# Optimization experiments

Hardware: AMD Instinct MI355X
Metric: run time of the kernel (lower is better)

## Reference

```python
import jax, jax.numpy as jnp
import numpy as np

IN_DIM = 1024
OUT_DIM = 1024
NHEAD = 16
K = 9  # template(1032) - dim(1024) + 1


def _slinear(vec, template, conv_w, conv_b, lin_b):
    # Conv2d over template produces the [out_dim, in_dim] weight matrix.
    w = jax.lax.conv_general_dilated(
        template, conv_w, window_strides=(1, 1), padding='VALID',
        dimension_numbers=('NCHW', 'OIHW', 'NCHW'))  # [1,1,out_dim,in_dim]
    w = w[0, 0] + conv_b  # broadcast conv bias (scalar per out-channel)
    return vec @ w.T + lin_b  # F.linear(vec, w) + bias


def setup_inputs() -> dict:
    key = jax.random.key(0)
    ks = jax.random.split(key, 13)
    S, B = 2048, 2
    d = {
        'query': jax.random.normal(ks[0], (S, B, IN_DIM), jnp.float32),
        'key': jax.random.normal(ks[1], (S, B, IN_DIM), jnp.float32),
        'value': jax.random.normal(ks[2], (S, B, IN_DIM), jnp.float32),
        'template': jax.random.normal(ks[3], (1, 1, 1032, 1032), jnp.float32),
    }
    for i, name in enumerate(['wq', 'wk', 'wv']):
        d[name + '_cw'] = jax.random.normal(ks[4 + 3 * i], (1, 1, K, K), jnp.float32) * 0.05
        d[name + '_cb'] = jax.random.normal(ks[5 + 3 * i], (1,), jnp.float32) * 0.05
        d[name + '_b'] = jax.random.normal(ks[6 + 3 * i], (OUT_DIM,), jnp.float32) * 0.05
    return d


def reference(query, key, value, template,
              wq_cw, wq_cb, wq_b, wk_cw, wk_cb, wk_b, wv_cw, wv_cb, wv_b):
    q = _slinear(query, template, wq_cw, wq_cb, wq_b)
    k = _slinear(key, template, wk_cw, wk_cb, wk_b)
    v = _slinear(value, template, wv_cw, wv_cb, wv_b)
    S, B = q.shape[0], q.shape[1]
    h_dim = OUT_DIM // NHEAD
    scale = h_dim ** 0.5
    qh = q.reshape(S, B, NHEAD, h_dim)
    kh = k.reshape(S, B, NHEAD, h_dim)
    vh = v.reshape(S, B, NHEAD, h_dim)
    # batch_first=False path: scores then softmax over last dim
    scores = jnp.einsum('ibhd,jbhd->bhij', qh, kh) / scale  # [B,H,S,S]
    attn = jax.nn.softmax(scores, axis=-1)
    out = jnp.einsum('bhij,jbhd->ibhd', attn, vh).reshape(S, B, OUT_DIM)
    return out
```

## Files before the change

kernel.cpp:

```cpp
#include <hip/hip_runtime.h>
#include <math.h>

#define TDIM   1032
#define DIM    1024
#define SLEN   2048
#define BATCH  2
#define NROWS  (SLEN*BATCH)
#define NHEAD  16
#define HD     64

typedef unsigned short u16;
typedef short short8 __attribute__((ext_vector_type(8)));
typedef short bf16x4 __attribute__((ext_vector_type(4)));
typedef float f32x4  __attribute__((ext_vector_type(4)));

#define CSCALE 0.18033688011112042f

__device__ inline unsigned fbits(float x) {
    union { float f; unsigned u; } v; v.f = x; return v.u;
}
__device__ inline float asfloat(unsigned u) {
    union { unsigned u; float f; } v; v.u = u; return v.f;
}
__device__ inline u16 f2bf_rne(float x) {
    unsigned u = fbits(x);
    unsigned r = u + 0x7fffu + ((u >> 16) & 1u);
    return (u16)(r >> 16);
}
__device__ inline float bf2f(u16 b) { return asfloat(((unsigned)b) << 16); }
__device__ inline void dma16(const u16* g, u16* l) {
    __builtin_amdgcn_global_load_lds(
        (const __attribute__((address_space(1))) void*)g,
        (__attribute__((address_space(3))) void*)l, 16, 0, 0);
}

__global__ __launch_bounds__(256) void conv_weight_kernel(
    const float* __restrict__ tmpl,
    const float* __restrict__ cw0, const float* __restrict__ cb0,
    const float* __restrict__ cw1, const float* __restrict__ cb1,
    const float* __restrict__ cw2, const float* __restrict__ cb2,
    u16* __restrict__ Wh, u16* __restrict__ Wl)
{
    int t = blockIdx.z;
    const float* cw = (t == 0) ? cw0 : ((t == 1) ? cw1 : cw2);
    const float* cb = (t == 0) ? cb0 : ((t == 1) ? cb1 : cb2);
    __shared__ float scw[81];
    if (threadIdx.x < 81) scw[threadIdx.x] = cw[threadIdx.x];
    __syncthreads();
    int i = blockIdx.x * 256 + threadIdx.x;
    int o4 = blockIdx.y * 4;
    float cbv = cb[0];
    float acc[4] = {cbv, cbv, cbv, cbv};
    #pragma unroll
    for (int ry = 0; ry < 12; ++ry) {
        const float* trow = tmpl + (size_t)(o4 + ry) * TDIM + i;
        float tv[9];
        #pragma unroll
        for (int dx = 0; dx < 9; ++dx) tv[dx] = trow[dx];
        #pragma unroll
        for (int oo = 0; oo < 4; ++oo) {
            int dy = ry - oo;
            if (dy >= 0 && dy <= 8) {
                #pragma unroll
                for (int dx = 0; dx < 9; ++dx)
                    acc[oo] = fmaf(scw[dy * 9 + dx], tv[dx], acc[oo]);
            }
        }
    }
    #pragma unroll
    for (int oo = 0; oo < 4; ++oo) {
        size_t idx = (size_t)t * DIM * DIM + (size_t)(o4 + oo) * DIM + i;
        u16 h = f2bf_rne(acc[oo]);
        Wh[idx] = h;
        Wl[idx] = f2bf_rne(acc[oo] - bf2f(h));
    }
}

__global__ __launch_bounds__(256, 3) void qkv_mfma_gemm(
    const float* __restrict__ x0, const float* __restrict__ x1,
    const float* __restrict__ x2,
    const u16* __restrict__ Whg, const u16* __restrict__ Wlg,
    const float* __restrict__ b0, const float* __restrict__ b1,
    const float* __restrict__ b2,
    u16* __restrict__ Qh, u16* __restrict__ Ql,
    u16* __restrict__ Kh, u16* __restrict__ Kl,
    u16* __restrict__ Vb)
{
    unsigned flat = blockIdx.x + 8u * blockIdx.y + 256u * blockIdx.z;
    unsigned swz = (flat & 7u) * 96u + (flat >> 3);
    int t = swz >> 8;
    int n0 = (swz & 7u) * 128;
    int m0 = ((swz >> 3) & 31u) * 128;

    const float* X    = (t == 0) ? x0 : ((t == 1) ? x1 : x2);
    const u16* Bh_g   = Whg + (size_t)t * DIM * DIM;
    const u16* Bl_g   = Wlg + (size_t)t * DIM * DIM;
    const float* bias = (t == 0) ? b0 : ((t == 1) ? b1 : b2);

    __shared__ __align__(16) u16 lds[16384];
    u16* sAh = lds;
    u16* sAl = lds + 4096;
    u16* sBh = lds + 8192;
    u16* sBl = lds + 12288;

    int tid = threadIdx.x;
    int w = tid >> 6, lane = tid & 63;
    int c = lane & 15, quad = lane >> 4;
    int mh = (w >> 1) * 64, nh = (w & 1) * 64;

    int arow = w * 32 + (lane & 31);
    int acol = (lane >> 5) * 16;
    const float* aptr = X + (size_t)(m0 + arow) * DIM + acol;

    int srow = lane >> 2, sgr = lane & 3;

    f32x4 acc[4][4];
    #pragma unroll
    for (int i = 0; i < 4; ++i)
        #pragma unroll
        for (int j = 0; j < 4; ++j)
            #pragma unroll
            for (int r = 0; r < 4; ++r) acc[i][j][r] = 0.0f;

    float bias_v[4];
    #pragma unroll
    for (int tn = 0; tn < 4; ++tn) bias_v[tn] = bias[n0 + nh + tn * 16 + c];

    float4 xa[4];
    #pragma unroll
    for (int i = 0; i < 2; ++i) {
        int rb = w * 32 + i * 16;
        const u16* gh = Bh_g + (size_t)(n0 + rb + srow) * DIM + sgr * 8;
        const u16* gl = Bl_g + (size_t)(n0 + rb + srow) * DIM + sgr * 8;
        dma16(gh, sBh + rb * 32);
        dma16(gl, sBl + rb * 32);
    }
    #pragma unroll
    for (int j = 0; j < 4; ++j) xa[j] = *(const float4*)(aptr + j * 4);

    for (int it = 0; it < 32; ++it) {
        #pragma unroll
        for (int g = 0; g < 2; ++g) {
            float v[8] = { xa[2*g].x, xa[2*g].y, xa[2*g].z, xa[2*g].w,
                           xa[2*g+1].x, xa[2*g+1].y, xa[2*g+1].z, xa[2*g+1].w };
            short8 hv, lv;
            #pragma unroll
            for (int e = 0; e < 8; ++e) {
                unsigned u = fbits(v[e]);
                hv[e] = (short)(u >> 16);
                float l = v[e] - asfloat(u & 0xffff0000u);
                lv[e] = (short)(fbits(l) >> 16);
            }
            *(short8*)(sAh + arow * 32 + acol + g * 8) = hv;
            *(short8*)(sAl + arow * 32 + acol + g * 8) = lv;
        }
        __syncthreads();

        short8 ah[4], al[4], bh[4], bl[4];
        #pragma unroll
        for (int tt = 0; tt < 4; ++tt) {
            int mi = (mh + tt * 16 + c) * 32 + quad * 8;
            ah[tt] = *(short8*)(sAh + mi);
            al[tt] = *(short8*)(sAl + mi);
            int ni = (nh + tt * 16 + c) * 32 + quad * 8;
            bh[tt] = *(short8*)(sBh + ni);
            bl[tt] = *(short8*)(sBl + ni);
        }
        __syncthreads();

        if (it < 31) {
            int kg = (it + 1) * 4;
            #pragma unroll
            for (int i = 0; i < 2; ++i) {
                int rb = w * 32 + i * 16;
                const u16* gh = Bh_g + (size_t)(n0 + rb + srow) * DIM + (kg + sgr) * 8;
                const u16* gl = Bl_g + (size_t)(n0 + rb + srow) * DIM + (kg + sgr) * 8;
                dma16(gh, sBh + rb * 32);
                dma16(gl, sBl + rb * 32);
            }
            #pragma unroll
            for (int j = 0; j < 4; ++j)
                xa[j] = *(const float4*)(aptr + (it + 1) * 32 + j * 4);
        }

        #pragma unroll
        for (int tm = 0; tm < 4; ++tm)
            #pragma unroll
            for (int tn = 0; tn < 4; ++tn) {
                acc[tm][tn] = __builtin_amdgcn_mfma_f32_16x16x32_bf16(
                    ah[tm], bh[tn], acc[tm][tn], 0, 0, 0);
                acc[tm][tn] = __builtin_amdgcn_mfma_f32_16x16x32_bf16(
                    ah[tm], bl[tn], acc[tm][tn], 0, 0, 0);
                acc[tm][tn] = __builtin_amdgcn_mfma_f32_16x16x32_bf16(
                    al[tm], bh[tn], acc[tm][tn], 0, 0, 0);
            }
    }

    if (t < 2) {
        u16* Yh = (t == 0) ? Qh : Kh;
        u16* Yl = (t == 0) ? Ql : Kl;
        float qs = (t == 0) ? CSCALE : 1.0f;
        #pragma unroll
        for (int tm = 0; tm < 4; ++tm)
            #pragma unroll
            for (int r = 0; r < 4; ++r) {
                int m = m0 + mh + tm * 16 + quad * 4 + r;
                #pragma unroll
                for (int tn = 0; tn < 4; ++tn) {
                    int n = n0 + nh + tn * 16 + c;
                    float o = (acc[tm][tn][r] + bias_v[tn]) * qs;
                    unsigned bo = fbits(o);
                    Yh[(size_t)m * DIM + n] = (u16)(bo >> 16);
                    float l = o - asfloat(bo & 0xffff0000u);
                    Yl[(size_t)m * DIM + n] = (u16)(fbits(l) >> 16);
                }
            }
    } else {
        #pragma unroll
        for (int tm = 0; tm < 4; ++tm)
            #pragma unroll
            for (int r = 0; r < 4; ++r) {
                int m = m0 + mh + tm * 16 + quad * 4 + r;
                #pragma unroll
                for (int tn = 0; tn < 4; ++tn) {
                    int n = n0 + nh + tn * 16 + c;
                    Vb[(size_t)m * DIM + n] =
                        (u16)(fbits(acc[tm][tn][r] + bias_v[tn]) >> 16);
                }
            }
    }
}

__global__ __launch_bounds__(256) void vt_kernel(
    const u16* __restrict__ Vb, u16* __restrict__ Vt)
{
    int b = blockIdx.z, h = blockIdx.y, s0 = blockIdx.x * 64;
    __shared__ __align__(16) u16 tile[64][80];
    int tid = threadIdx.x;
    int sl = tid >> 2, d0 = (tid & 3) * 16;
    const u16* src = Vb + (size_t)((s0 + sl) * BATCH + b) * DIM + h * HD + d0;
    short8 v0 = *(const short8*)src;
    short8 v1 = *(const short8*)(src + 8);
    #pragma unroll
    for (int j = 0; j < 8; ++j) {
        tile[d0 + j][sl] = (u16)v0[j];
        tile[d0 + 8 + j][sl] = (u16)v1[j];
    }
    __syncthreads();
    int d = tid >> 2, sc0 = (tid & 3) * 16;
    u16* dst = Vt + (size_t)((b * NHEAD + h) * HD + d) * SLEN + s0 + sc0;
    *(short8*)dst = *(const short8*)&tile[d][sc0];
    *(short8*)(dst + 8) = *(const short8*)&tile[d][sc0 + 8];
}

__global__ __launch_bounds__(256, 3) void attn_mfma_kernel(
    const u16* __restrict__ Qh, const u16* __restrict__ Ql,
    const u16* __restrict__ Kh, const u16* __restrict__ Kl,
    const u16* __restrict__ Vt, float* __restrict__ out)
{
    unsigned flat = blockIdx.x + 16u * blockIdx.y + 256u * blockIdx.z;
    unsigned swz = (flat & 7u) * 64u + (flat >> 3);
    int q0 = (swz & 15u) * 128;
    int h = (swz >> 4) & 15u;
    int b = swz >> 8;

    int tid = threadIdx.x;
    int w = tid >> 6, lane = tid & 63;
    int c = lane & 15, quad = lane >> 4;

    __shared__ __align__(16) u16 sbuf[2][3][4096];

    short8 qhf[2][2], qlf[2][2];
    #pragma unroll
    for (int u = 0; u < 2; ++u) {
        int s = q0 + w * 32 + u * 16 + c;
        size_t base = (size_t)(s * BATCH + b) * DIM + h * HD + quad * 8;
        qhf[u][0] = *(const short8*)(Qh + base);
        qhf[u][1] = *(const short8*)(Qh + base + 32);
        qlf[u][0] = *(const short8*)(Ql + base);
        qlf[u][1] = *(const short8*)(Ql + base + 32);
    }

    f32x4 acc[2][4];
    #pragma unroll
    for (int u = 0; u < 2; ++u)
        #pragma unroll
        for (int i = 0; i < 4; ++i)
            #pragma unroll
            for (int r = 0; r < 4; ++r) acc[u][i][r] = 0.0f;
    float m_run[2] = {-1e38f, -1e38f}, l_run[2] = {0.0f, 0.0f};

    int r3 = lane >> 3, c3 = lane & 7;
    int sw = c3 ^ r3;
    const size_t bhofs = (size_t)(b * NHEAD + h) * HD;

    #define ISSUE_DMA(n0v, bufv) do {                                          \
        _Pragma("unroll")                                                      \
        for (int j = 0; j < 2; ++j) {                                          \
            int i_ = 2 * w + j;                                                \
            int row_ = i_ * 8 + r3;                                            \
            size_t gk = (size_t)(((n0v) + row_) * BATCH + b) * DIM + h * HD + sw * 8; \
            dma16(Kh + gk, &sbuf[bufv][0][i_ * 512]);                          \
            dma16(Kl + gk, &sbuf[bufv][1][i_ * 512]);                          \
            size_t gv = (bhofs + row_) * SLEN + (n0v) + sw * 8;                \
            dma16(Vt + gv, &sbuf[bufv][2][i_ * 512]);                          \
        }                                                                      \
    } while (0)

    ISSUE_DMA(0, 0);

    for (int it = 0; it < 32; ++it) {
        int cur = it & 1;
        __syncthreads();
        if (it < 31) ISSUE_DMA((it + 1) * 64, cur ^ 1);

        const u16* bKh = sbuf[cur][0];
        const u16* bKl = sbuf[cur][1];
        const u16* bVt = sbuf[cur][2];

        f32x4 sc[2][4];
        #pragma unroll
        for (int ct = 0; ct < 4; ++ct) {
            int row = ct * 16 + c, rw = row & 7;
            int kb = row * 64;
            short8 kh0 = *(const short8*)(bKh + kb + ((quad ^ rw) * 8));
            short8 kh1 = *(const short8*)(bKh + kb + (((4 + quad) ^ rw) * 8));
            short8 kl0 = *(const short8*)(bKl + kb + ((quad ^ rw) * 8));
            short8 kl1 = *(const short8*)(bKl + kb + (((4 + quad) ^ rw) * 8));
            __builtin_amdgcn_s_setprio(1);
            #pragma unroll
            for (int u = 0; u < 2; ++u) {
                f32x4 s = {0.0f, 0.0f, 0.0f, 0.0f};
                s = __builtin_amdgcn_mfma_f32_16x16x32_bf16(kh0, qhf[u][0], s, 0, 0, 0);
                s = __builtin_amdgcn_mfma_f32_16x16x32_bf16(kh1, qhf[u][1], s, 0, 0, 0);
                s = __builtin_amdgcn_mfma_f32_16x16x32_bf16(kh0, qlf[u][0], s, 0, 0, 0);
                s = __builtin_amdgcn_mfma_f32_16x16x32_bf16(kh1, qlf[u][1], s, 0, 0, 0);
                s = __builtin_amdgcn_mfma_f32_16x16x32_bf16(kl0, qhf[u][0], s, 0, 0, 0);
                s = __builtin_amdgcn_mfma_f32_16x16x32_bf16(kl1, qhf[u][1], s, 0, 0, 0);
                sc[u][ct] = s;
            }
            __builtin_amdgcn_s_setprio(0);
        }

        short8 pf[2][2];
        #pragma unroll
        for (int u = 0; u < 2; ++u) {
            float pm = sc[u][0][0];
            #pragma unroll
            for (int ct = 0; ct < 4; ++ct)
                #pragma unroll
                for (int r = 0; r < 4; ++r)
                    pm = fmaxf(pm, sc[u][ct][r]);
            pm = fmaxf(pm, __shfl_xor(pm, 16));
            pm = fmaxf(pm, __shfl_xor(pm, 32));
            float mnew = fmaxf(m_run[u], pm);
            bool noresc = __all(pm <= m_run[u]);
            if (!noresc) {
                float al = exp2f(m_run[u] - mnew);
                float alr[4];
                #pragma unroll
                for (int r = 0; r < 4; ++r)
                    alr[r] = __shfl(al, (lane & 48) | (quad * 4 + r));
                #pragma unroll
                for (int ctd = 0; ctd < 4; ++ctd)
                    #pragma unroll
                    for (int r = 0; r < 4; ++r) acc[u][ctd][r] *= alr[r];
                l_run[u] *= al;
            }
            m_run[u] = mnew;

            float ps = 0.0f;
            unsigned pw[8];
            #pragma unroll
            for (int ct = 0; ct < 4; ++ct) {
                float p0 = exp2f(sc[u][ct][0] - mnew);
                float p1 = exp2f(sc[u][ct][1] - mnew);
                float p2 = exp2f(sc[u][ct][2] - mnew);
                float p3 = exp2f(sc[u][ct][3] - mnew);
                ps += (p0 + p1) + (p2 + p3);
                pw[2*ct]   = (fbits(p0) >> 16) | (fbits(p1) & 0xffff0000u);
                pw[2*ct+1] = (fbits(p2) >> 16) | (fbits(p3) & 0xffff0000u);
            }
            ps += __shfl_xor(ps, 16);
            ps += __shfl_xor(ps, 32);
            l_run[u] += ps;

            int sl0 = c + ((quad & 1) << 5);
            int sl1 = sl0 + 16;
            int sel = quad >> 1;
            union W8 { unsigned wv[4]; short8 s8; } f0, f1;
            {
                unsigned a0 = __shfl(pw[0], sl0), a1 = __shfl(pw[2], sl0);
                f0.wv[0] = sel ? a1 : a0;
                unsigned b0 = __shfl(pw[1], sl0), b1 = __shfl(pw[3], sl0);
                f0.wv[1] = sel ? b1 : b0;
                unsigned c0 = __shfl(pw[0], sl1), c1 = __shfl(pw[2], sl1);
                f0.wv[2] = sel ? c1 : c0;
                unsigned d0 = __shfl(pw[1], sl1), d1 = __shfl(pw[3], sl1);
                f0.wv[3] = sel ? d1 : d0;
                unsigned e0 = __shfl(pw[4], sl0), e1 = __shfl(pw[6], sl0);
                f1.wv[0] = sel ? e1 : e0;
                unsigned g0 = __shfl(pw[5], sl0), g1 = __shfl(pw[7], sl0);
                f1.wv[1] = sel ? g1 : g0;
                unsigned h0 = __shfl(pw[4], sl1), h1 = __shfl(pw[6], sl1);
                f1.wv[2] = sel ? h1 : h0;
                unsigned i0 = __shfl(pw[5], sl1), i1 = __shfl(pw[7], sl1);
                f1.wv[3] = sel ? i1 : i0;
            }
            pf[u][0] = f0.s8;
            pf[u][1] = f1.s8;
        }

        #pragma unroll
        for (int ctd = 0; ctd < 4; ++ctd) {
            int vrow = ctd * 16 + c, vrw = vrow & 7;
            int vb = vrow * 64;
            short8 v0 = *(const short8*)(bVt + vb + ((quad ^ vrw) * 8));
            short8 v1 = *(const short8*)(bVt + vb + (((4 + quad) ^ vrw) * 8));
            __builtin_amdgcn_s_setprio(1);
            #pragma unroll
            for (int u = 0; u < 2; ++u) {
                acc[u][ctd] = __builtin_amdgcn_mfma_f32_16x16x32_bf16(
                    pf[u][0], v0, acc[u][ctd], 0, 0, 0);
                acc[u][ctd] = __builtin_amdgcn_mfma_f32_16x16x32_bf16(
                    pf[u][1], v1, acc[u][ctd], 0, 0, 0);
            }
            __builtin_amdgcn_s_setprio(0);
        }
    }
    #undef ISSUE_DMA

    #pragma unroll
    for (int u = 0; u < 2; ++u) {
        float rl[4];
        #pragma unroll
        for (int r = 0; r < 4; ++r)
            rl[r] = 1.0f / __shfl(l_run[u], (lane & 48) | (quad * 4 + r));
        #pragma unroll
        for (int ctd = 0; ctd < 4; ++ctd)
            #pragma unroll
            for (int r = 0; r < 4; ++r) {
                int s = q0 + w * 32 + u * 16 + quad * 4 + r;
                out[(size_t)(s * BATCH + b) * DIM + h * HD + ctd * 16 + c] =
                    acc[u][ctd][r] * rl[r];
            }
    }
}

extern "C" void kernel_launch(void* const* d_in, const int* in_sizes, int n_in,
                              void* d_out, int out_size, void* d_ws, size_t ws_size,
                              hipStream_t stream)
{
    const float* query = (const float*)d_in[0];
    const float* key_  = (const float*)d_in[1];
    const float* value = (const float*)d_in[2];
    const float* tmpl  = (const float*)d_in[3];
    const float* wq_cw = (const float*)d_in[4];
    const float* wq_cb = (const float*)d_in[5];
    const float* wq_b  = (const float*)d_in[6];
    const float* wk_cw = (const float*)d_in[7];
    const float* wk_cb = (const float*)d_in[8];
    const float* wk_b  = (const float*)d_in[9];
    const float* wv_cw = (const float*)d_in[10];
    const float* wv_cb = (const float*)d_in[11];
    const float* wv_b  = (const float*)d_in[12];

    char* ws = (char*)d_ws;
    u16* Wh = (u16*)(ws);
    u16* Wl = (u16*)(ws + 6291456);
    u16* Qh = (u16*)(ws + 12582912);
    u16* Ql = (u16*)(ws + 20971520);
    u16* Kh = (u16*)(ws + 29360128);
    u16* Kl = (u16*)(ws + 37748736);
    u16* Vb = (u16*)(ws + 46137344);
    u16* Vt = (u16*)(ws + 54525952);
    float* out = (float*)d_out;

    conv_weight_kernel<<<dim3(DIM / 256, DIM / 4, 3), 256, 0, stream>>>(
        tmpl, wq_cw, wq_cb, wk_cw, wk_cb, wv_cw, wv_cb, Wh, Wl);

    qkv_mfma_gemm<<<dim3(DIM / 128, NROWS / 128, 3), 256, 0, stream>>>(
        query, key_, value, Wh, Wl, wq_b, wk_b, wv_b, Qh, Ql, Kh, Kl, Vb);

    vt_kernel<<<dim3(SLEN / 64, NHEAD, BATCH), 256, 0, stream>>>(Vb, Vt);

    attn_mfma_kernel<<<dim3(SLEN / 128, NHEAD, BATCH), 256, 0, stream>>>(
        Qh, Ql, Kh, Kl, Vt, out);
}
```

Baseline: 321.7 us.

## Use 8 waves per attention block with 16 query rows each

The attention kernel now launches 512 threads per block, so each of 8 waves handles a single 16-row query tile instead of two. Each wave issues one K/V DMA chunk instead of two, and all V fragments are loaded from LDS before the softmax so the PV MFMAs run back to back under raised priority. This lowers per-thread register use to allow more waves per CU and better latency hiding. In exchange, each K/V fragment read from LDS now feeds fewer MFMAs, and the barrier spans more waves.

```diff
diff --git a/kernel.cpp b/kernel.cpp
--- a/kernel.cpp
+++ b/kernel.cpp
@@ -253,7 +253,7 @@
     *(short8*)(dst + 8) = *(const short8*)&tile[d][sc0 + 8];
 }
 
-__global__ __launch_bounds__(256, 3) void attn_mfma_kernel(
+__global__ __launch_bounds__(512, 4) void attn_mfma_kernel(
     const u16* __restrict__ Qh, const u16* __restrict__ Ql,
     const u16* __restrict__ Kh, const u16* __restrict__ Kl,
     const u16* __restrict__ Vt, float* __restrict__ out)
@@ -270,41 +270,34 @@
 
     __shared__ __align__(16) u16 sbuf[2][3][4096];
 
-    short8 qhf[2][2], qlf[2][2];
-    #pragma unroll
-    for (int u = 0; u < 2; ++u) {
-        int s = q0 + w * 32 + u * 16 + c;
+    short8 qhf[2], qlf[2];
+    {
+        int s = q0 + w * 16 + c;
         size_t base = (size_t)(s * BATCH + b) * DIM + h * HD + quad * 8;
-        qhf[u][0] = *(const short8*)(Qh + base);
-        qhf[u][1] = *(const short8*)(Qh + base + 32);
-        qlf[u][0] = *(const short8*)(Ql + base);
-        qlf[u][1] = *(const short8*)(Ql + base + 32);
-    }
-
-    f32x4 acc[2][4];
-    #pragma unroll
-    for (int u = 0; u < 2; ++u)
-        #pragma unroll
-        for (int i = 0; i < 4; ++i)
-            #pragma unroll
-            for (int r = 0; r < 4; ++r) acc[u][i][r] = 0.0f;
-    float m_run[2] = {-1e38f, -1e38f}, l_run[2] = {0.0f, 0.0f};
+        qhf[0] = *(const short8*)(Qh + base);
+        qhf[1] = *(const short8*)(Qh + base + 32);
+        qlf[0] = *(const short8*)(Ql + base);
+        qlf[1] = *(const short8*)(Ql + base + 32);
+    }
+
+    f32x4 acc[4];
+    #pragma unroll
+    for (int i = 0; i < 4; ++i)
+        #pragma unroll
+        for (int r = 0; r < 4; ++r) acc[i][r] = 0.0f;
+    float m_run = -1e38f, l_run = 0.0f;
 
     int r3 = lane >> 3, c3 = lane & 7;
     int sw = c3 ^ r3;
     const size_t bhofs = (size_t)(b * NHEAD + h) * HD;
 
     #define ISSUE_DMA(n0v, bufv) do {                                          \
-        _Pragma("unroll")                                                      \
-        for (int j = 0; j < 2; ++j) {                                          \
-            int i_ = 2 * w + j;                                                \
-            int row_ = i_ * 8 + r3;                                            \
-            size_t gk = (size_t)(((n0v) + row_) * BATCH + b) * DIM + h * HD + sw * 8; \
-            dma16(Kh + gk, &sbuf[bufv][0][i_ * 512]);                          \
-            dma16(Kl + gk, &sbuf[bufv][1][i_ * 512]);                          \
-            size_t gv = (bhofs + row_) * SLEN + (n0v) + sw * 8;                \
-            dma16(Vt + gv, &sbuf[bufv][2][i_ * 512]);                          \
-        }                                                                      \
+        int row_ = w * 8 + r3;                                                 \
+        size_t gk = (size_t)(((n0v) + row_) * BATCH + b) * DIM + h * HD + sw * 8; \
+        dma16(Kh + gk, &sbuf[bufv][0][w * 512]);                               \
+        dma16(Kl + gk, &sbuf[bufv][1][w * 512]);                               \
+        size_t gv = (bhofs + row_) * SLEN + (n0v) + sw * 8;                    \
+        dma16(Vt + gv, &sbuf[bufv][2][w * 512]);                               \
     } while (0)
 
     ISSUE_DMA(0, 0);
@@ -318,7 +311,7 @@
         const u16* bKl = sbuf[cur][1];
         const u16* bVt = sbuf[cur][2];
 
-        f32x4 sc[2][4];
+        f32x4 sc[4];
         #pragma unroll
         for (int ct = 0; ct < 4; ++ct) {
             int row = ct * 16 + c, rw = row & 7;
@@ -328,35 +321,40 @@
             short8 kl0 = *(const short8*)(bKl + kb + ((quad ^ rw) * 8));
             short8 kl1 = *(const short8*)(bKl + kb + (((4 + quad) ^ rw) * 8));
             __builtin_amdgcn_s_setprio(1);
-            #pragma unroll
-            for (int u = 0; u < 2; ++u) {
-                f32x4 s = {0.0f, 0.0f, 0.0f, 0.0f};
-                s = __builtin_amdgcn_mfma_f32_16x16x32_bf16(kh0, qhf[u][0], s, 0, 0, 0);
-                s = __builtin_amdgcn_mfma_f32_16x16x32_bf16(kh1, qhf[u][1], s, 0, 0, 0);
-                s = __builtin_amdgcn_mfma_f32_16x16x32_bf16(kh0, qlf[u][0], s, 0, 0, 0);
-                s = __builtin_amdgcn_mfma_f32_16x16x32_bf16(kh1, qlf[u][1], s, 0, 0, 0);
-                s = __builtin_amdgcn_mfma_f32_16x16x32_bf16(kl0, qhf[u][0], s, 0, 0, 0);
-                s = __builtin_amdgcn_mfma_f32_16x16x32_bf16(kl1, qhf[u][1], s, 0, 0, 0);
-                sc[u][ct] = s;
-            }
+            f32x4 s = {0.0f, 0.0f, 0.0f, 0.0f};
+            s = __builtin_amdgcn_mfma_f32_16x16x32_bf16(kh0, qhf[0], s, 0, 0, 0);
+            s = __builtin_amdgcn_mfma_f32_16x16x32_bf16(kh1, qhf[1], s, 0, 0, 0);
+            s = __builtin_amdgcn_mfma_f32_16x16x32_bf16(kh0, qlf[0], s, 0, 0, 0);
+            s = __builtin_amdgcn_mfma_f32_16x16x32_bf16(kh1, qlf[1], s, 0, 0, 0);
+            s = __builtin_amdgcn_mfma_f32_16x16x32_bf16(kl0, qhf[0], s, 0, 0, 0);
+            s = __builtin_amdgcn_mfma_f32_16x16x32_bf16(kl1, qhf[1], s, 0, 0, 0);
             __builtin_amdgcn_s_setprio(0);
-        }
-
-        short8 pf[2][2];
-        #pragma unroll
-        for (int u = 0; u < 2; ++u) {
-            float pm = sc[u][0][0];
+            sc[ct] = s;
+        }
+
+        short8 vv[4][2];
+        #pragma unroll
+        for (int ctd = 0; ctd < 4; ++ctd) {
+            int vrow = ctd * 16 + c, vrw = vrow & 7;
+            int vb = vrow * 64;
+            vv[ctd][0] = *(const short8*)(bVt + vb + ((quad ^ vrw) * 8));
+            vv[ctd][1] = *(const short8*)(bVt + vb + (((4 + quad) ^ vrw) * 8));
+        }
+
+        short8 pf0, pf1;
+        {
+            float pm = sc[0][0];
             #pragma unroll
             for (int ct = 0; ct < 4; ++ct)
                 #pragma unroll
                 for (int r = 0; r < 4; ++r)
-                    pm = fmaxf(pm, sc[u][ct][r]);
+                    pm = fmaxf(pm, sc[ct][r]);
             pm = fmaxf(pm, __shfl_xor(pm, 16));
             pm = fmaxf(pm, __shfl_xor(pm, 32));
-            float mnew = fmaxf(m_run[u], pm);
-            bool noresc = __all(pm <= m_run[u]);
+            float mnew = fmaxf(m_run, pm);
+            bool noresc = __all(pm <= m_run);
             if (!noresc) {
-                float al = exp2f(m_run[u] - mnew);
+                float al = exp2f(m_run - mnew);
                 float alr[4];
                 #pragma unroll
                 for (int r = 0; r < 4; ++r)
@@ -364,26 +362,26 @@
                 #pragma unroll
                 for (int ctd = 0; ctd < 4; ++ctd)
                     #pragma unroll
-                    for (int r = 0; r < 4; ++r) acc[u][ctd][r] *= alr[r];
-                l_run[u] *= al;
-            }
-            m_run[u] = mnew;
+                    for (int r = 0; r < 4; ++r) acc[ctd][r] *= alr[r];
+                l_run *= al;
+            }
+            m_run = mnew;
 
             float ps = 0.0f;
             unsigned pw[8];
             #pragma unroll
             for (int ct = 0; ct < 4; ++ct) {
-                float p0 = exp2f(sc[u][ct][0] - mnew);
-                float p1 = exp2f(sc[u][ct][1] - mnew);
-                float p2 = exp2f(sc[u][ct][2] - mnew);
-                float p3 = exp2f(sc[u][ct][3] - mnew);
+                float p0 = exp2f(sc[ct][0] - mnew);
+                float p1 = exp2f(sc[ct][1] - mnew);
+                float p2 = exp2f(sc[ct][2] - mnew);
+                float p3 = exp2f(sc[ct][3] - mnew);
                 ps += (p0 + p1) + (p2 + p3);
                 pw[2*ct]   = (fbits(p0) >> 16) | (fbits(p1) & 0xffff0000u);
                 pw[2*ct+1] = (fbits(p2) >> 16) | (fbits(p3) & 0xffff0000u);
             }
             ps += __shfl_xor(ps, 16);
             ps += __shfl_xor(ps, 32);
-            l_run[u] += ps;
+            l_run += ps;
 
             int sl0 = c + ((quad & 1) << 5);
             int sl1 = sl0 + 16;
@@ -407,42 +405,34 @@
                 unsigned i0 = __shfl(pw[5], sl1), i1 = __shfl(pw[7], sl1);
                 f1.wv[3] = sel ? i1 : i0;
             }
-            pf[u][0] = f0.s8;
-            pf[u][1] = f1.s8;
-        }
-
+            pf0 = f0.s8;
+            pf1 = f1.s8;
+        }
+
+        __builtin_amdgcn_s_setprio(1);
         #pragma unroll
         for (int ctd = 0; ctd < 4; ++ctd) {
-            int vrow = ctd * 16 + c, vrw = vrow & 7;
-            int vb = vrow * 64;
-            short8 v0 = *(const short8*)(bVt + vb + ((quad ^ vrw) * 8));
-            short8 v1 = *(const short8*)(bVt + vb + (((4 + quad) ^ vrw) * 8));
-            __builtin_amdgcn_s_setprio(1);
-            #pragma unroll
-            for (int u = 0; u < 2; ++u) {
-                acc[u][ctd] = __builtin_amdgcn_mfma_f32_16x16x32_bf16(
-                    pf[u][0], v0, acc[u][ctd], 0, 0, 0);
-                acc[u][ctd] = __builtin_amdgcn_mfma_f32_16x16x32_bf16(
-                    pf[u][1], v1, acc[u][ctd], 0, 0, 0);
-            }
-            __builtin_amdgcn_s_setprio(0);
-        }
+            acc[ctd] = __builtin_amdgcn_mfma_f32_16x16x32_bf16(
+                pf0, vv[ctd][0], acc[ctd], 0, 0, 0);
+            acc[ctd] = __builtin_amdgcn_mfma_f32_16x16x32_bf16(
+                pf1, vv[ctd][1], acc[ctd], 0, 0, 0);
+        }
+        __builtin_amdgcn_s_setprio(0);
     }
     #undef ISSUE_DMA
 
-    #pragma unroll
-    for (int u = 0; u < 2; ++u) {
+    {
         float rl[4];
         #pragma unroll
         for (int r = 0; r < 4; ++r)
-            rl[r] = 1.0f / __shfl(l_run[u], (lane & 48) | (quad * 4 + r));
+            rl[r] = 1.0f / __shfl(l_run, (lane & 48) | (quad * 4 + r));
         #pragma unroll
         for (int ctd = 0; ctd < 4; ++ctd)
             #pragma unroll
             for (int r = 0; r < 4; ++r) {
-                int s = q0 + w * 32 + u * 16 + quad * 4 + r;
+                int s = q0 + w * 16 + quad * 4 + r;
                 out[(size_t)(s * BATCH + b) * DIM + h * HD + ctd * 16 + c] =
-                    acc[u][ctd][r] * rl[r];
+                    acc[ctd][r] * rl[r];
             }
     }
 }
@@ -484,6 +474,6 @@
 
     vt_kernel<<<dim3(SLEN / 64, NHEAD, BATCH), 256, 0, stream>>>(Vb, Vt);
 
-    attn_mfma_kernel<<<dim3(SLEN / 128, NHEAD, BATCH), 256, 0, stream>>>(
+    attn_mfma_kernel<<<dim3(SLEN / 128, NHEAD, BATCH), 512, 0, stream>>>(
         Qh, Ql, Kh, Kl, Vt, out);
 }
```

Result: faster. 311.8 us (-3.1%).
